# Kernel tuning notes

Measured on AMD Instinct MI355X. Metric: run time of the kernel, lower is better.

The kernel has to match this reference:

```python
import jax, jax.numpy as jnp
import numpy as np

NUM_NODES = 100000
EMBED_DIM = 128
NUM_RELATIONS = 64
BATCH = 512


def setup_inputs() -> dict:
    key = jax.random.key(0)
    k1, k2, k3, k4, k5 = jax.random.split(key, 5)
    u = jax.random.randint(k1, (BATCH,), 0, NUM_NODES)
    v = jax.random.randint(k2, (BATCH,), 0, NUM_NODES)
    r = jax.random.randint(k3, (BATCH,), 0, NUM_RELATIONS)
    node_embeddings = jax.random.normal(k4, (NUM_NODES, EMBED_DIM), dtype=jnp.float32)
    relation_matrices = jax.random.normal(k5, (NUM_RELATIONS, EMBED_DIM, EMBED_DIM), dtype=jnp.float32)
    return {"u": u, "v": v, "r": r,
            "node_embeddings": node_embeddings,
            "relation_matrices": relation_matrices}


def reference(u, v, r, node_embeddings, relation_matrices):
    u_embed = node_embeddings[u]            # [B, D]
    v_embed = node_embeddings[v]            # [B, D]
    rel = relation_matrices[r]              # [B, D, D] per-sample gathered matrices
    # torch.matmul([B,D], [B,D,D]) broadcasts u_embed over the relation batch -> [B_rel, B_u, D]
    score = jnp.einsum('ud,bde->bue', u_embed, rel)   # [B, B, D]
    # matmul with v_embed.T [D, B] -> [B, B, B]
    score = jnp.einsum('bue,ve->buv', score, v_embed)  # [B, B, B]
    return jax.nn.sigmoid(score)
```

## Files before the change

kernel.cpp:

```cpp
#include <hip/hip_runtime.h>


#define BATCH 512
#define DIM   128
#define NRELS 64
#define UTILE 64
#define VTILE 64
#define NTHR  256

typedef float floatx4 __attribute__((ext_vector_type(4)));

__global__ __launch_bounds__(NTHR, 2)
void rad_fused_kernel(const int* __restrict__ u_idx,
                      const int* __restrict__ v_idx,
                      const int* __restrict__ r_idx,
                      const float* __restrict__ nodes,
                      const float* __restrict__ rels,
                      float* __restrict__ out)
{
    const int rel = (int)blockIdx.x >> 3;
    const int ut0 = ((int)blockIdx.x & 7) * UTILE;

    __shared__ int s_match[BATCH];
    __shared__ int s_mc;
    __shared__ __align__(16) float s_TsT[DIM * UTILE];
    __shared__ __align__(16) float s_buf[DIM * UTILE + 16 * DIM];

    const int t  = (int)threadIdx.x;
    const int tu = t >> 4;
    const int tx = t & 15;

    if (t == 0) s_mc = 0;
    __syncthreads();
    for (int i = t; i < BATCH; i += NTHR) {
        if (r_idx[i] == rel) {
            int p = atomicAdd(&s_mc, 1);
            s_match[p] = i;
        }
    }

    float* UEsT = s_buf;
    float* Rs   = s_buf + DIM * UTILE;

    for (int i = t; i < UTILE * (DIM / 4); i += NTHR) {
        const int row = i & (UTILE - 1);
        const int dc  = i >> 6;
        const float4 val = *reinterpret_cast<const float4*>(
            nodes + (size_t)u_idx[ut0 + row] * DIM + dc * 4);
        UEsT[(dc * 4 + 0) * UTILE + row] = val.x;
        UEsT[(dc * 4 + 1) * UTILE + row] = val.y;
        UEsT[(dc * 4 + 2) * UTILE + row] = val.z;
        UEsT[(dc * 4 + 3) * UTILE + row] = val.w;
    }
    __syncthreads();
    const int mc = s_mc;
    if (mc == 0) return;

    float accA[4][8];
    #pragma unroll
    for (int i = 0; i < 4; ++i)
        #pragma unroll
        for (int j = 0; j < 8; ++j) accA[i][j] = 0.f;

    const float* Rbase = rels + (size_t)rel * DIM * DIM;
    for (int dch = 0; dch < DIM / 16; ++dch) {
        for (int i = t; i < 16 * (DIM / 4); i += NTHR) {
            const int rr = i >> 5;
            const int cc = i & 31;
            *reinterpret_cast<float4*>(Rs + rr * DIM + cc * 4) =
                *reinterpret_cast<const float4*>(
                    Rbase + (size_t)(dch * 16 + rr) * DIM + cc * 4);
        }
        __syncthreads();
        #pragma unroll
        for (int dd = 0; dd < 16; ++dd) {
            const int d = dch * 16 + dd;
            const float4 a  = *reinterpret_cast<const float4*>(UEsT + d * UTILE + tu * 4);
            const float4 b0 = *reinterpret_cast<const float4*>(Rs + dd * DIM + tx * 4);
            const float4 b1 = *reinterpret_cast<const float4*>(Rs + dd * DIM + 64 + tx * 4);
            const float av[4] = {a.x, a.y, a.z, a.w};
            const float bv[8] = {b0.x, b0.y, b0.z, b0.w, b1.x, b1.y, b1.z, b1.w};
            #pragma unroll
            for (int i = 0; i < 4; ++i)
                #pragma unroll
                for (int j = 0; j < 8; ++j)
                    accA[i][j] = fmaf(av[i], bv[j], accA[i][j]);
        }
        __syncthreads();
    }

    #pragma unroll
    for (int j = 0; j < 8; ++j) {
        const int e = (j < 4) ? (tx * 4 + j) : (64 + tx * 4 + (j - 4));
        #pragma unroll
        for (int i = 0; i < 4; ++i)
            s_TsT[e * UTILE + tu * 4 + i] = accA[i][j];
    }

    float* VEsT = s_buf;
    for (int vt = 0; vt < BATCH / VTILE; ++vt) {
        __syncthreads();
        for (int i = t; i < VTILE * (DIM / 4); i += NTHR) {
            const int row = i & (VTILE - 1);
            const int ec  = i >> 6;
            const float4 val = *reinterpret_cast<const float4*>(
                nodes + (size_t)v_idx[vt * VTILE + row] * DIM + ec * 4);
            VEsT[(ec * 4 + 0) * VTILE + row] = val.x;
            VEsT[(ec * 4 + 1) * VTILE + row] = val.y;
            VEsT[(ec * 4 + 2) * VTILE + row] = val.z;
            VEsT[(ec * 4 + 3) * VTILE + row] = val.w;
        }
        __syncthreads();

        float acc[4][4];
        #pragma unroll
        for (int i = 0; i < 4; ++i)
            #pragma unroll
            for (int j = 0; j < 4; ++j) acc[i][j] = 0.f;

        #pragma unroll 8
        for (int e = 0; e < DIM; ++e) {
            const float4 a = *reinterpret_cast<const float4*>(s_TsT + e * UTILE + tu * 4);
            const float4 b = *reinterpret_cast<const float4*>(VEsT  + e * VTILE + tx * 4);
            const float av[4] = {a.x, a.y, a.z, a.w};
            const float bv[4] = {b.x, b.y, b.z, b.w};
            #pragma unroll
            for (int i = 0; i < 4; ++i)
                #pragma unroll
                for (int j = 0; j < 4; ++j)
                    acc[i][j] = fmaf(av[i], bv[j], acc[i][j]);
        }

        floatx4 sg[4];
        #pragma unroll
        for (int i = 0; i < 4; ++i) {
            sg[i].x = 1.f / (1.f + __expf(-acc[i][0]));
            sg[i].y = 1.f / (1.f + __expf(-acc[i][1]));
            sg[i].z = 1.f / (1.f + __expf(-acc[i][2]));
            sg[i].w = 1.f / (1.f + __expf(-acc[i][3]));
        }

        for (int m = 0; m < mc; ++m) {
            const int bb = s_match[m];
            float* obase = out + (size_t)bb * BATCH * BATCH;
            #pragma unroll
            for (int i = 0; i < 4; ++i) {
                floatx4* dst = reinterpret_cast<floatx4*>(
                    obase + (size_t)(ut0 + tu * 4 + i) * BATCH + vt * VTILE + tx * 4);
                __builtin_nontemporal_store(sg[i], dst);
            }
        }
    }
}

extern "C" void kernel_launch(void* const* d_in, const int* in_sizes, int n_in,
                              void* d_out, int out_size, void* d_ws, size_t ws_size,
                              hipStream_t stream) {
    const int*   u_idx = (const int*)d_in[0];
    const int*   v_idx = (const int*)d_in[1];
    const int*   r_idx = (const int*)d_in[2];
    const float* nodes = (const float*)d_in[3];
    const float* rels  = (const float*)d_in[4];
    float* out = (float*)d_out;

    dim3 grid(NRELS * (BATCH / UTILE));
    dim3 block(NTHR);
    rad_fused_kernel<<<grid, block, 0, stream>>>(u_idx, v_idx, r_idx, nodes, rels, out);
}
```

Before: 144.5 us.

## Split fused kernel into relation-transform and scoring phases via workspace

Adds a first kernel that computes the per-relation transformed u-embeddings T = U·R_rel and writes them to a global workspace. A second kernel then runs one block per (relation, u-tile, v-tile), so the grid grows from 512 to 4096 blocks. Each block computes its 64x64 score tile, applies the sigmoid and writes it to every matching batch slot. The aim is more parallelism and better overlap of the dominant output writes. In exchange it adds a second launch, a workspace write and read, and it computes T for relations with no matching batch entries. The original fused kernel stays as a fallback when the workspace is too small.

```diff
diff --git a/kernel.cpp b/kernel.cpp
--- a/kernel.cpp
+++ b/kernel.cpp
@@ -4,11 +4,174 @@
 #define BATCH 512
 #define DIM   128
 #define NRELS 64
-#define UTILE 64
-#define VTILE 64
 #define NTHR  256
 
 typedef float floatx4 __attribute__((ext_vector_type(4)));
+
+__global__ __launch_bounds__(NTHR, 4)
+void rad_phaseA_kernel(const int* __restrict__ u_idx,
+                       const float* __restrict__ nodes,
+                       const float* __restrict__ rels,
+                       float* __restrict__ T_ws)
+{
+    const int rel = (int)blockIdx.x >> 3;
+    const int ut0 = ((int)blockIdx.x & 7) * 64;
+
+    __shared__ __align__(16) float UEsT[DIM * 64];
+    __shared__ __align__(16) float Rs[16 * DIM];
+
+    const int t  = (int)threadIdx.x;
+    const int tu = t >> 4;
+    const int tx = t & 15;
+
+    for (int i = t; i < 64 * (DIM / 4); i += NTHR) {
+        const int row = i & 63;
+        const int dc  = i >> 6;
+        const float4 val = *reinterpret_cast<const float4*>(
+            nodes + (size_t)u_idx[ut0 + row] * DIM + dc * 4);
+        UEsT[(dc * 4 + 0) * 64 + row] = val.x;
+        UEsT[(dc * 4 + 1) * 64 + row] = val.y;
+        UEsT[(dc * 4 + 2) * 64 + row] = val.z;
+        UEsT[(dc * 4 + 3) * 64 + row] = val.w;
+    }
+
+    float accA[4][8];
+    #pragma unroll
+    for (int i = 0; i < 4; ++i)
+        #pragma unroll
+        for (int j = 0; j < 8; ++j) accA[i][j] = 0.f;
+
+    const float* Rbase = rels + (size_t)rel * DIM * DIM;
+    for (int dch = 0; dch < DIM / 16; ++dch) {
+        __syncthreads();
+        for (int i = t; i < 16 * (DIM / 4); i += NTHR) {
+            const int rr = i >> 5;
+            const int cc = i & 31;
+            *reinterpret_cast<float4*>(Rs + rr * DIM + cc * 4) =
+                *reinterpret_cast<const float4*>(
+                    Rbase + (size_t)(dch * 16 + rr) * DIM + cc * 4);
+        }
+        __syncthreads();
+        #pragma unroll
+        for (int dd = 0; dd < 16; ++dd) {
+            const int d = dch * 16 + dd;
+            const float4 a  = *reinterpret_cast<const float4*>(UEsT + d * 64 + tu * 4);
+            const float4 b0 = *reinterpret_cast<const float4*>(Rs + dd * DIM + tx * 4);
+            const float4 b1 = *reinterpret_cast<const float4*>(Rs + dd * DIM + 64 + tx * 4);
+            const float av[4] = {a.x, a.y, a.z, a.w};
+            const float bv[8] = {b0.x, b0.y, b0.z, b0.w, b1.x, b1.y, b1.z, b1.w};
+            #pragma unroll
+            for (int i = 0; i < 4; ++i)
+                #pragma unroll
+                for (int j = 0; j < 8; ++j)
+                    accA[i][j] = fmaf(av[i], bv[j], accA[i][j]);
+        }
+    }
+
+    #pragma unroll
+    for (int i = 0; i < 4; ++i) {
+        float* rowp = T_ws + ((size_t)rel * BATCH + ut0 + tu * 4 + i) * DIM;
+        *reinterpret_cast<float4*>(rowp + tx * 4) =
+            make_float4(accA[i][0], accA[i][1], accA[i][2], accA[i][3]);
+        *reinterpret_cast<float4*>(rowp + 64 + tx * 4) =
+            make_float4(accA[i][4], accA[i][5], accA[i][6], accA[i][7]);
+    }
+}
+
+__global__ __launch_bounds__(NTHR, 2)
+void rad_phaseB_kernel(const int* __restrict__ v_idx,
+                       const int* __restrict__ r_idx,
+                       const float* __restrict__ nodes,
+                       const float* __restrict__ T_ws,
+                       float* __restrict__ out)
+{
+    const int bid = (int)blockIdx.x;
+    const int rel = bid >> 6;
+    const int ut0 = ((bid >> 3) & 7) * 64;
+    const int vt0 = (bid & 7) * 64;
+
+    __shared__ int s_match[BATCH];
+    __shared__ int s_mc;
+    __shared__ __align__(16) float TsT[DIM * 64];
+    __shared__ __align__(16) float VEsT[DIM * 64];
+
+    const int t  = (int)threadIdx.x;
+    const int tu = t >> 4;
+    const int tx = t & 15;
+
+    if (t == 0) s_mc = 0;
+    __syncthreads();
+    for (int i = t; i < BATCH; i += NTHR) {
+        if (r_idx[i] == rel) {
+            int p = atomicAdd(&s_mc, 1);
+            s_match[p] = i;
+        }
+    }
+    __syncthreads();
+    const int mc = s_mc;
+    if (mc == 0) return;
+
+    for (int i = t; i < 64 * (DIM / 4); i += NTHR) {
+        const int row = i & 63;
+        const int ec  = i >> 6;
+        const float4 val = *reinterpret_cast<const float4*>(
+            T_ws + ((size_t)rel * BATCH + ut0 + row) * DIM + ec * 4);
+        TsT[(ec * 4 + 0) * 64 + row] = val.x;
+        TsT[(ec * 4 + 1) * 64 + row] = val.y;
+        TsT[(ec * 4 + 2) * 64 + row] = val.z;
+        TsT[(ec * 4 + 3) * 64 + row] = val.w;
+    }
+    for (int i = t; i < 64 * (DIM / 4); i += NTHR) {
+        const int row = i & 63;
+        const int ec  = i >> 6;
+        const float4 val = *reinterpret_cast<const float4*>(
+            nodes + (size_t)v_idx[vt0 + row] * DIM + ec * 4);
+        VEsT[(ec * 4 + 0) * 64 + row] = val.x;
+        VEsT[(ec * 4 + 1) * 64 + row] = val.y;
+        VEsT[(ec * 4 + 2) * 64 + row] = val.z;
+        VEsT[(ec * 4 + 3) * 64 + row] = val.w;
+    }
+    __syncthreads();
+
+    float acc[4][4];
+    #pragma unroll
+    for (int i = 0; i < 4; ++i)
+        #pragma unroll
+        for (int j = 0; j < 4; ++j) acc[i][j] = 0.f;
+
+    #pragma unroll 8
+    for (int e = 0; e < DIM; ++e) {
+        const float4 a = *reinterpret_cast<const float4*>(TsT  + e * 64 + tu * 4);
+        const float4 b = *reinterpret_cast<const float4*>(VEsT + e * 64 + tx * 4);
+        const float av[4] = {a.x, a.y, a.z, a.w};
+        const float bv[4] = {b.x, b.y, b.z, b.w};
+        #pragma unroll
+        for (int i = 0; i < 4; ++i)
+            #pragma unroll
+            for (int j = 0; j < 4; ++j)
+                acc[i][j] = fmaf(av[i], bv[j], acc[i][j]);
+    }
+
+    floatx4 sg[4];
+    #pragma unroll
+    for (int i = 0; i < 4; ++i) {
+        sg[i].x = 1.f / (1.f + __expf(-acc[i][0]));
+        sg[i].y = 1.f / (1.f + __expf(-acc[i][1]));
+        sg[i].z = 1.f / (1.f + __expf(-acc[i][2]));
+        sg[i].w = 1.f / (1.f + __expf(-acc[i][3]));
+    }
+
+    for (int m = 0; m < mc; ++m) {
+        const int bb = s_match[m];
+        float* obase = out + (size_t)bb * BATCH * BATCH;
+        #pragma unroll
+        for (int i = 0; i < 4; ++i) {
+            floatx4* dst = reinterpret_cast<floatx4*>(
+                obase + (size_t)(ut0 + tu * 4 + i) * BATCH + vt0 + tx * 4);
+            __builtin_nontemporal_store(sg[i], dst);
+        }
+    }
+}
 
 __global__ __launch_bounds__(NTHR, 2)
 void rad_fused_kernel(const int* __restrict__ u_idx,
@@ -19,12 +182,12 @@
                       float* __restrict__ out)
 {
     const int rel = (int)blockIdx.x >> 3;
-    const int ut0 = ((int)blockIdx.x & 7) * UTILE;
+    const int ut0 = ((int)blockIdx.x & 7) * 64;
 
     __shared__ int s_match[BATCH];
     __shared__ int s_mc;
-    __shared__ __align__(16) float s_TsT[DIM * UTILE];
-    __shared__ __align__(16) float s_buf[DIM * UTILE + 16 * DIM];
+    __shared__ __align__(16) float s_TsT[DIM * 64];
+    __shared__ __align__(16) float s_buf[DIM * 64 + 16 * DIM];
 
     const int t  = (int)threadIdx.x;
     const int tu = t >> 4;
@@ -40,17 +203,17 @@
     }
 
     float* UEsT = s_buf;
-    float* Rs   = s_buf + DIM * UTILE;
-
-    for (int i = t; i < UTILE * (DIM / 4); i += NTHR) {
-        const int row = i & (UTILE - 1);
+    float* Rs   = s_buf + DIM * 64;
+
+    for (int i = t; i < 64 * (DIM / 4); i += NTHR) {
+        const int row = i & 63;
         const int dc  = i >> 6;
         const float4 val = *reinterpret_cast<const float4*>(
             nodes + (size_t)u_idx[ut0 + row] * DIM + dc * 4);
-        UEsT[(dc * 4 + 0) * UTILE + row] = val.x;
-        UEsT[(dc * 4 + 1) * UTILE + row] = val.y;
-        UEsT[(dc * 4 + 2) * UTILE + row] = val.z;
-        UEsT[(dc * 4 + 3) * UTILE + row] = val.w;
+        UEsT[(dc * 4 + 0) * 64 + row] = val.x;
+        UEsT[(dc * 4 + 1) * 64 + row] = val.y;
+        UEsT[(dc * 4 + 2) * 64 + row] = val.z;
+        UEsT[(dc * 4 + 3) * 64 + row] = val.w;
     }
     __syncthreads();
     const int mc = s_mc;
@@ -75,7 +238,7 @@
         #pragma unroll
         for (int dd = 0; dd < 16; ++dd) {
             const int d = dch * 16 + dd;
-            const float4 a  = *reinterpret_cast<const float4*>(UEsT + d * UTILE + tu * 4);
+            const float4 a  = *reinterpret_cast<const float4*>(UEsT + d * 64 + tu * 4);
             const float4 b0 = *reinterpret_cast<const float4*>(Rs + dd * DIM + tx * 4);
             const float4 b1 = *reinterpret_cast<const float4*>(Rs + dd * DIM + 64 + tx * 4);
             const float av[4] = {a.x, a.y, a.z, a.w};
@@ -94,21 +257,21 @@
         const int e = (j < 4) ? (tx * 4 + j) : (64 + tx * 4 + (j - 4));
         #pragma unroll
         for (int i = 0; i < 4; ++i)
-            s_TsT[e * UTILE + tu * 4 + i] = accA[i][j];
+            s_TsT[e * 64 + tu * 4 + i] = accA[i][j];
     }
 
     float* VEsT = s_buf;
-    for (int vt = 0; vt < BATCH / VTILE; ++vt) {
-        __syncthreads();
-        for (int i = t; i < VTILE * (DIM / 4); i += NTHR) {
-            const int row = i & (VTILE - 1);
+    for (int vt = 0; vt < BATCH / 64; ++vt) {
+        __syncthreads();
+        for (int i = t; i < 64 * (DIM / 4); i += NTHR) {
+            const int row = i & 63;
             const int ec  = i >> 6;
             const float4 val = *reinterpret_cast<const float4*>(
-                nodes + (size_t)v_idx[vt * VTILE + row] * DIM + ec * 4);
-            VEsT[(ec * 4 + 0) * VTILE + row] = val.x;
-            VEsT[(ec * 4 + 1) * VTILE + row] = val.y;
-            VEsT[(ec * 4 + 2) * VTILE + row] = val.z;
-            VEsT[(ec * 4 + 3) * VTILE + row] = val.w;
+                nodes + (size_t)v_idx[vt * 64 + row] * DIM + ec * 4);
+            VEsT[(ec * 4 + 0) * 64 + row] = val.x;
+            VEsT[(ec * 4 + 1) * 64 + row] = val.y;
+            VEsT[(ec * 4 + 2) * 64 + row] = val.z;
+            VEsT[(ec * 4 + 3) * 64 + row] = val.w;
         }
         __syncthreads();
 
@@ -120,8 +283,8 @@
 
         #pragma unroll 8
         for (int e = 0; e < DIM; ++e) {
-            const float4 a = *reinterpret_cast<const float4*>(s_TsT + e * UTILE + tu * 4);
-            const float4 b = *reinterpret_cast<const float4*>(VEsT  + e * VTILE + tx * 4);
+            const float4 a = *reinterpret_cast<const float4*>(s_TsT + e * 64 + tu * 4);
+            const float4 b = *reinterpret_cast<const float4*>(VEsT  + e * 64 + tx * 4);
             const float av[4] = {a.x, a.y, a.z, a.w};
             const float bv[4] = {b.x, b.y, b.z, b.w};
             #pragma unroll
@@ -146,7 +309,7 @@
             #pragma unroll
             for (int i = 0; i < 4; ++i) {
                 floatx4* dst = reinterpret_cast<floatx4*>(
-                    obase + (size_t)(ut0 + tu * 4 + i) * BATCH + vt * VTILE + tx * 4);
+                    obase + (size_t)(ut0 + tu * 4 + i) * BATCH + vt * 64 + tx * 4);
                 __builtin_nontemporal_store(sg[i], dst);
             }
         }
@@ -163,7 +326,15 @@
     const float* rels  = (const float*)d_in[4];
     float* out = (float*)d_out;
 
-    dim3 grid(NRELS * (BATCH / UTILE));
-    dim3 block(NTHR);
-    rad_fused_kernel<<<grid, block, 0, stream>>>(u_idx, v_idx, r_idx, nodes, rels, out);
+    const size_t t_bytes = (size_t)NRELS * BATCH * DIM * sizeof(float);
+    if (ws_size >= t_bytes) {
+        float* T_ws = (float*)d_ws;
+        rad_phaseA_kernel<<<dim3(NRELS * 8), dim3(NTHR), 0, stream>>>(
+            u_idx, nodes, rels, T_ws);
+        rad_phaseB_kernel<<<dim3(NRELS * 8 * 8), dim3(NTHR), 0, stream>>>(
+            v_idx, r_idx, nodes, T_ws, out);
+    } else {
+        rad_fused_kernel<<<dim3(NRELS * 8), dim3(NTHR), 0, stream>>>(
+            u_idx, v_idx, r_idx, nodes, rels, out);
+    }
 }
```

Measured after the change: 157.3 us. 8.9% more time.
